# Performance work log

Measured on AMD Instinct MI355X. Metric: run time of the kernel, lower is better.

Reference implementation:

```python
import jax, jax.numpy as jnp
import numpy as np

L, B, D, N = 4096, 8, 1024, 16


def setup_inputs() -> dict:
    key = jax.random.key(0)
    ks = jax.random.split(key, 6)
    # ema_expansion_matrix init: alternating +-1 plus small noise (per reset_parameters)
    sign = jnp.where(jnp.arange(N) % 2 == 1, -1.0, 1.0)[None, :, None]
    return {
        "x": jax.random.normal(ks[0], (L, B, D), dtype=jnp.float32),
        "damping_factor": 0.2 * jax.random.normal(ks[1], (D, N, 1), dtype=jnp.float32),
        "decay_factor": 0.2 * jax.random.normal(ks[2], (D, N, 1), dtype=jnp.float32),
        "ema_expansion_matrix": sign + 0.02 * jax.random.normal(ks[3], (D, N, 1), dtype=jnp.float32),
        "kernel_projection_matrix": jax.random.normal(ks[4], (D, N), dtype=jnp.float32),
        "residual_weight": jax.random.normal(ks[5], (D,), dtype=jnp.float32),
    }


def reference(x, damping_factor, decay_factor, ema_expansion_matrix,
              kernel_projection_matrix, residual_weight):
    # x: (L, B, D)
    length = x.shape[0]
    num_heads = damping_factor.shape[1]
    scaling = (1.0 / num_heads) ** 0.5

    residual = x * residual_weight  # (L, B, D)
    xc = jnp.transpose(x, (1, 2, 0))  # (B, D, L)

    # EMA coefficients
    p = jax.nn.sigmoid(damping_factor)                     # (D, N, 1)
    q = 1.0 - p * jax.nn.sigmoid(decay_factor)             # (D, N, 1)

    # Vandermonde kernel: (D, N, L) -> project to (D, L)
    t = jnp.arange(length, dtype=x.dtype)[None, None, :]
    kernel_dnl = p * ema_expansion_matrix * jnp.exp(t * jnp.log(q))
    kernel = jnp.einsum('dnl,dn->dl', kernel_dnl, kernel_projection_matrix * scaling)

    # Causal FFT convolution with n = 2L
    n_fft = 2 * length
    k_f = jnp.fft.rfft(kernel, n=n_fft)                    # (D, n/2+1)
    x_f = jnp.fft.rfft(xc, n=n_fft)                        # (B, D, n/2+1)
    out = jnp.fft.irfft(x_f * k_f, n=n_fft)[..., :length]  # (B, D, L)

    out = jnp.transpose(out, (2, 0, 1)) + residual         # (L, B, D)
    return jax.nn.relu(out)
```

## Files before the change

kernel.cpp:

```cpp
#include <hip/hip_runtime.h>
#include <math.h>

#define L 4096
#define B 8
#define D 1024
#define NH 16
#define COUT 128
#define WB 128
#define NCHUNK (L / COUT)
#define BD 8192

#define REP16(F) F(0) F(1) F(2) F(3) F(4) F(5) F(6) F(7) F(8) F(9) F(10) F(11) F(12) F(13) F(14) F(15)
#define REP8(F)  F(0) F(1) F(2) F(3) F(4) F(5) F(6) F(7)

__device__ __forceinline__ float sigmoidf(float v) {
    return 1.0f / (1.0f + __expf(-v));
}

#define UPD(i) s##i = fmaf(q##i, s##i, xv);
#define UPDALL UPD(0) UPD(1) UPD(2) UPD(3) UPD(4) UPD(5) UPD(6) UPD(7) \
               UPD(8) UPD(9) UPD(10) UPD(11) UPD(12) UPD(13) UPD(14) UPD(15)
#define ACC(i) s##i = fmaf(q##i, s##i, xv); y = fmaf(P##i, s##i, y);
#define ACCALL ACC(0) ACC(1) ACC(2) ACC(3) ACC(4) ACC(5) ACC(6) ACC(7) \
               ACC(8) ACC(9) ACC(10) ACC(11) ACC(12) ACC(13) ACC(14) ACC(15)

__global__ void __launch_bounds__(256, 4)
ema_fused(const float* __restrict__ x,
          const float* __restrict__ damp,
          const float* __restrict__ decay,
          const float* __restrict__ ema,
          const float* __restrict__ proj,
          const float* __restrict__ rw,
          float* __restrict__ out) {
    int d = blockIdx.x * 256 + threadIdx.x;
    int c = blockIdx.y;
    int b = blockIdx.z;

    const float* dp = damp  + d * NH;
    const float* dc = decay + d * NH;
    const float* de = ema   + d * NH;
    const float* pj = proj  + d * NH;

#define DECLQS(i) float q##i, s##i;
    REP16(DECLQS)
#define INITQS(i) { q##i = 1.0f - sigmoidf(dp[i]) * sigmoidf(dc[i]); s##i = 0.0f; }
    REP16(INITQS)

    const size_t base = (size_t)b * D + d;

    if (c > 0) {
        const float* xp = x + (size_t)(c * COUT - WB) * BD + base;
#define LDA16(i) float a##i = xp[i * BD];
        REP16(LDA16)
        xp += 16 * BD;
        for (int r = 0; r < WB - 16; r += 16) {
#define LDB16(i) float t##i = xp[i * BD];
            REP16(LDB16)
            xp += 16 * BD;
#define CONS16(i) { float xv = a##i; UPDALL }
            REP16(CONS16)
#define MOV16(i) a##i = t##i;
            REP16(MOV16)
        }
        REP16(CONS16)
    }

#define DECLP(i) float P##i;
    REP16(DECLP)
#define INITP(i) { float p_ = sigmoidf(dp[i]); P##i = p_ * de[i] * pj[i] * 0.25f; }
    REP16(INITP)
    float w = rw[d];

    const float* xp = x   + (size_t)(c * COUT) * BD + base;
    float*       op = out + (size_t)(c * COUT) * BD + base;

#define EMIT(v, k) { float xv = (v); float y = xv * w; ACCALL \
                     __builtin_nontemporal_store(fmaxf(y, 0.0f), op + (k) * BD); }

#define LDA8(i) float a##i = xp[i * BD];
    REP8(LDA8)
    xp += 8 * BD;
    for (int r = 0; r < COUT - 8; r += 8) {
#define LDB8(i) float t##i = xp[i * BD];
        REP8(LDB8)
        xp += 8 * BD;
#define EM8(i) EMIT(a##i, i)
        REP8(EM8)
        op += 8 * BD;
#define MOV8(i) a##i = t##i;
        REP8(MOV8)
    }
    REP8(EM8)
}

extern "C" void kernel_launch(void* const* d_in, const int* in_sizes, int n_in,
                              void* d_out, int out_size, void* d_ws, size_t ws_size,
                              hipStream_t stream) {
    const float* x     = (const float*)d_in[0];
    const float* damp  = (const float*)d_in[1];
    const float* decay = (const float*)d_in[2];
    const float* ema   = (const float*)d_in[3];
    const float* proj  = (const float*)d_in[4];
    const float* rw    = (const float*)d_in[5];
    float* out = (float*)d_out;

    dim3 grid(D / 256, NCHUNK, B);
    ema_fused<<<grid, 256, 0, stream>>>(x, damp, decay, ema, proj, rw, out);
}
```

Baseline: 298.9 us.

## Split the 16 EMA heads across lane pairs and combine with a shuffle

Each channel's 16 EMA states are now divided between two adjacent lanes, 8 heads each. The partial outputs are summed with a xor-shuffle and only the even lane stores. This halves per-thread serial FMA work and register use and doubles the thread count, so occupancy can rise (launch bounds go to 8 blocks per SM). In exchange every x element is loaded redundantly by both lanes, each output step adds a shuffle, and half the lanes sit idle during stores, which makes the store pattern less dense.

After: 307.3 us. +2.8%, slower.

```diff
diff --git a/kernel.cpp b/kernel.cpp
--- a/kernel.cpp
+++ b/kernel.cpp
@@ -18,13 +18,11 @@
 }
 
 #define UPD(i) s##i = fmaf(q##i, s##i, xv);
-#define UPDALL UPD(0) UPD(1) UPD(2) UPD(3) UPD(4) UPD(5) UPD(6) UPD(7) \
-               UPD(8) UPD(9) UPD(10) UPD(11) UPD(12) UPD(13) UPD(14) UPD(15)
+#define UPDALL UPD(0) UPD(1) UPD(2) UPD(3) UPD(4) UPD(5) UPD(6) UPD(7)
 #define ACC(i) s##i = fmaf(q##i, s##i, xv); y = fmaf(P##i, s##i, y);
-#define ACCALL ACC(0) ACC(1) ACC(2) ACC(3) ACC(4) ACC(5) ACC(6) ACC(7) \
-               ACC(8) ACC(9) ACC(10) ACC(11) ACC(12) ACC(13) ACC(14) ACC(15)
+#define ACCALL ACC(0) ACC(1) ACC(2) ACC(3) ACC(4) ACC(5) ACC(6) ACC(7)
 
-__global__ void __launch_bounds__(256, 4)
+__global__ void __launch_bounds__(256, 8)
 ema_fused(const float* __restrict__ x,
           const float* __restrict__ damp,
           const float* __restrict__ decay,
@@ -32,19 +30,24 @@
           const float* __restrict__ proj,
           const float* __restrict__ rw,
           float* __restrict__ out) {
-    int d = blockIdx.x * 256 + threadIdx.x;
-    int c = blockIdx.y;
-    int b = blockIdx.z;
+    const int tid  = threadIdx.x;
+    const int lane = tid & 63;
+    const int wv   = tid >> 6;
+    const int h    = lane & 1;
+    const int dl   = lane >> 1;
+    const int d    = blockIdx.x * 128 + wv * 32 + dl;
+    const int c    = blockIdx.y;
+    const int b    = blockIdx.z;
 
-    const float* dp = damp  + d * NH;
-    const float* dc = decay + d * NH;
-    const float* de = ema   + d * NH;
-    const float* pj = proj  + d * NH;
+    const float* dp = damp  + d * NH + h * 8;
+    const float* dc = decay + d * NH + h * 8;
+    const float* de = ema   + d * NH + h * 8;
+    const float* pj = proj  + d * NH + h * 8;
 
 #define DECLQS(i) float q##i, s##i;
-    REP16(DECLQS)
+    REP8(DECLQS)
 #define INITQS(i) { q##i = 1.0f - sigmoidf(dp[i]) * sigmoidf(dc[i]); s##i = 0.0f; }
-    REP16(INITQS)
+    REP8(INITQS)
 
     const size_t base = (size_t)b * D + d;
 
@@ -66,16 +69,17 @@
     }
 
 #define DECLP(i) float P##i;
-    REP16(DECLP)
+    REP8(DECLP)
 #define INITP(i) { float p_ = sigmoidf(dp[i]); P##i = p_ * de[i] * pj[i] * 0.25f; }
-    REP16(INITP)
-    float w = rw[d];
+    REP8(INITP)
+    const float weff = (h == 0) ? rw[d] : 0.0f;
 
     const float* xp = x   + (size_t)(c * COUT) * BD + base;
     float*       op = out + (size_t)(c * COUT) * BD + base;
 
-#define EMIT(v, k) { float xv = (v); float y = xv * w; ACCALL \
-                     __builtin_nontemporal_store(fmaxf(y, 0.0f), op + (k) * BD); }
+#define EMIT(v, k) { float xv = (v); float y = xv * weff; ACCALL \
+                     y += __shfl_xor(y, 1); \
+                     if (h == 0) __builtin_nontemporal_store(fmaxf(y, 0.0f), op + (k) * BD); }
 
 #define LDA8(i) float a##i = xp[i * BD];
     REP8(LDA8)
@@ -104,6 +108,6 @@
     const float* rw    = (const float*)d_in[5];
     float* out = (float*)d_out;
 
-    dim3 grid(D / 256, NCHUNK, B);
+    dim3 grid(D / 128, NCHUNK, B);
     ema_fused<<<grid, 256, 0, stream>>>(x, damp, decay, ema, proj, rw, out);
 }
```
